# Performance work log

Measured on AMD Instinct MI355X. Metric: run time of the kernel, lower is better.

## Reference

```python
import jax, jax.numpy as jnp
import numpy as np

# Static taxonomy layout (closed over; mirrors __init__ args La/layers)
LAYER_SIZES = (100, 1000, 5000, 13900)
LAYER_STARTS = tuple(int(s) for s in np.cumsum((0,) + LAYER_SIZES)[:-1])
N_NODES = int(sum(LAYER_SIZES))
H = len(LAYER_SIZES)
BATCH = 4096


def setup_inputs() -> dict:
    key = jax.random.key(0)
    y_pred = jax.random.normal(key, (BATCH, N_NODES), dtype=jnp.float32)

    rng = np.random.default_rng(0)
    # parents[v] = global index of v's parent in the previous layer
    parents = np.zeros(N_NODES, np.int32)
    for l in range(1, H):
        s, n = LAYER_STARTS[l], LAYER_SIZES[l]
        ps, pn = LAYER_STARTS[l - 1], LAYER_SIZES[l - 1]
        parents[s:s + n] = rng.integers(ps, ps + pn, size=n)

    # hierarchy-consistent one-hot targets: pick a leaf, mark it and all ancestors
    leaf = rng.integers(LAYER_STARTS[H - 1], N_NODES, size=BATCH)
    y_true = np.zeros((BATCH, N_NODES), np.float32)
    node = leaf
    rows = np.arange(BATCH)
    for l in range(H - 1, 0, -1):
        y_true[rows, node] = 1.0
        node = parents[node]
    y_true[rows, node] = 1.0  # layer-0 ancestor

    alpha_layer = jnp.array([0.0, 1.0, 1.0, 1.0], dtype=jnp.float32)
    return {
        "y_pred": y_pred,
        "y_true": jnp.asarray(y_true),
        "parents": jnp.asarray(parents),
        "alpha_layer": alpha_layer,
    }


def reference(y_pred, y_true, parents, alpha_layer):
    # Fused, batched version of the per-sample / per-layer Python loops.
    loss = jnp.float32(0.0)
    for l in range(1, H):  # small static loop over taxonomy layers
        s, n = LAYER_STARTS[l], LAYER_SIZES[l]
        ps, pn = LAYER_STARTS[l - 1], LAYER_SIZES[l - 1]

        logits = y_pred[:, s:s + n]                      # [B, n_l]
        p = jax.nn.softmax(logits, axis=1)               # outer softmax (as in source)
        # nn.CrossEntropyLoss with probability targets == -sum(t * log_softmax(input));
        # the source feeds the already-softmaxed p (double softmax) -> reproduce exactly.
        cce = -jnp.sum(y_true[:, s:s + n] * jax.nn.log_softmax(p, axis=1), axis=1)  # [B]

        # hierarchical dependency: child prob must not exceed its parent's prob
        pp = jax.nn.softmax(y_pred[:, ps:ps + pn], axis=1)   # [B, n_{l-1}]
        pidx = parents[s:s + n] - ps                         # local parent ids [n_l]
        d = jnp.mean(jax.nn.relu(p - pp[:, pidx]), axis=1)   # [B]

        loss = loss + jnp.mean(cce + d) * alpha_layer[l]
    return loss
```

## Files before the change

kernel.cpp:

```cpp
#include <hip/hip_runtime.h>
#include <math.h>

#define BATCH   4096
#define N_NODES 20000
#define H       4
#define BLOCK   512
#define NW      (BLOCK / 64)

__device__ __forceinline__ float waveSum(float v) {
#pragma unroll
    for (int off = 32; off > 0; off >>= 1) v += __shfl_xor(v, off);
    return v;
}

__device__ __forceinline__ float bf2f(ushort h) {
    return __uint_as_float(((unsigned)h) << 16);
}
__device__ __forceinline__ ushort f2bf_trunc(float x) {
    return (ushort)(__float_as_uint(x) >> 16);
}

__global__ __launch_bounds__(BLOCK, 8) void tax_main(
    const float* __restrict__ y_pred,
    const float* __restrict__ y_true,
    const int*   __restrict__ parents,
    const float* __restrict__ alpha,
    float*       __restrict__ partial)
{
    constexpr int LSTART[H] = {0, 100, 1100, 6100};
    constexpr int LSIZE[H]  = {100, 1000, 5000, 13900};

    __shared__ __align__(8) ushort row_bf[N_NODES];
    __shared__ float sc[NW * 13 + 16];
    __shared__ float invZ_s[H];
    __shared__ float aD_s[H];
    __shared__ float contrib_s[H];

    const int tid = threadIdx.x;
    const int b   = blockIdx.x;
    const int wid = tid >> 6;
    const int lid = tid & 63;

    const float4* yp4 = reinterpret_cast<const float4*>(y_pred + (size_t)b * N_NODES);
    const float4* yt4 = reinterpret_cast<const float4*>(y_true + (size_t)b * N_NODES);

#pragma unroll
    for (int l = 0; l < H; ++l) {
        const int sq = LSTART[l] / 4, nq = LSIZE[l] / 4;
        float z = 0.f, q2 = 0.f, dt = 0.f, ys = 0.f;
        for (int i = tid; i < nq; i += BLOCK) {
            float4 v = yp4[sq + i];
            float e0 = __expf(v.x), e1 = __expf(v.y);
            float e2 = __expf(v.z), e3 = __expf(v.w);
            ushort4 h;
            h.x = f2bf_trunc(e0); h.y = f2bf_trunc(e1);
            h.z = f2bf_trunc(e2); h.w = f2bf_trunc(e3);
            *reinterpret_cast<ushort4*>(&row_bf[4 * (sq + i)]) = h;
            z += (e0 + e1) + (e2 + e3);
            if (l > 0) {
                q2 += (e0 * e0 + e1 * e1) + (e2 * e2 + e3 * e3);
                float4 t = yt4[sq + i];
                dt += t.x * e0 + t.y * e1 + t.z * e2 + t.w * e3;
                ys += (t.x + t.y) + (t.z + t.w);
            }
        }
        z = waveSum(z);
        if (l > 0) { q2 = waveSum(q2); dt = waveSum(dt); ys = waveSum(ys); }
        if (lid == 0) {
            if (l == 0) {
                sc[wid * 13] = z;
            } else {
                float* p = &sc[wid * 13 + 1 + (l - 1) * 4];
                p[0] = z; p[1] = q2; p[2] = dt; p[3] = ys;
            }
        }
    }
    __syncthreads();

    if (tid < H) {
        const int l = tid;
        float z = 0.f, q2 = 0.f, dt = 0.f, ys = 0.f;
        if (l == 0) {
            for (int w = 0; w < NW; ++w) z += sc[w * 13];
        } else {
            for (int w = 0; w < NW; ++w) {
                const float* p = &sc[w * 13 + 1 + (l - 1) * 4];
                z += p[0]; q2 += p[1]; dt += p[2]; ys += p[3];
            }
        }
        float invZ = 1.f / z;
        invZ_s[l] = invZ;
        float al = alpha[l];
        if (l > 0) {
            float S = (float)(LSIZE[l] + 1) + 0.5f * q2 * invZ * invZ;
            contrib_s[l] = al * (logf(S) * ys - dt * invZ);
        } else {
            contrib_s[l] = 0.f;
        }
        aD_s[l] = al / (float)LSIZE[l];
    }
    __syncthreads();

#pragma unroll
    for (int l = 1; l < H; ++l) {
        const int s = LSTART[l], nq = LSIZE[l] / 4;
        const float invZ  = invZ_s[l];
        const float invZp = invZ_s[l - 1];
        const int4* pa4 = reinterpret_cast<const int4*>(parents + s);

        float D = 0.f;
        for (int i = tid; i < nq; i += BLOCK) {
            ushort4 h  = *reinterpret_cast<const ushort4*>(&row_bf[s + 4 * i]);
            int4    pa = pa4[i];
            float p0 = bf2f(h.x) * invZ;
            float p1 = bf2f(h.y) * invZ;
            float p2 = bf2f(h.z) * invZ;
            float p3 = bf2f(h.w) * invZ;
            float pp0 = bf2f(row_bf[pa.x]) * invZp;
            float pp1 = bf2f(row_bf[pa.y]) * invZp;
            float pp2 = bf2f(row_bf[pa.z]) * invZp;
            float pp3 = bf2f(row_bf[pa.w]) * invZp;
            D += fmaxf(p0 - pp0, 0.f) + fmaxf(p1 - pp1, 0.f)
               + fmaxf(p2 - pp2, 0.f) + fmaxf(p3 - pp3, 0.f);
        }
        D = waveSum(D);
        if (lid == 0) sc[wid * 4 + (l - 1)] = D;
    }
    __syncthreads();

    if (tid == 0) {
        float loss = contrib_s[1] + contrib_s[2] + contrib_s[3];
#pragma unroll
        for (int l = 1; l < H; ++l) {
            float Dl = 0.f;
            for (int w = 0; w < NW; ++w) Dl += sc[w * 4 + (l - 1)];
            loss += aD_s[l] * Dl;
        }
        partial[b] = loss;
    }
}

__global__ __launch_bounds__(1024) void tax_reduce(
    const float* __restrict__ partial, float* __restrict__ out)
{
    __shared__ float red[16];
    const int tid = threadIdx.x, wid = tid >> 6, lid = tid & 63;
    float v = 0.f;
    for (int i = tid; i < BATCH; i += 1024) v += partial[i];
    v = waveSum(v);
    if (lid == 0) red[wid] = v;
    __syncthreads();
    if (wid == 0) {
        float x = (lid < 16) ? red[lid] : 0.f;
        x = waveSum(x);
        if (lid == 0) out[0] = x * (1.0f / (float)BATCH);
    }
}

extern "C" void kernel_launch(void* const* d_in, const int* in_sizes, int n_in,
                              void* d_out, int out_size, void* d_ws, size_t ws_size,
                              hipStream_t stream) {
    const float* y_pred  = (const float*)d_in[0];
    const float* y_true  = (const float*)d_in[1];
    const int*   parents = (const int*)d_in[2];
    const float* alpha   = (const float*)d_in[3];
    float* partial = (float*)d_ws;
    float* out     = (float*)d_out;

    tax_main<<<dim3(BATCH), dim3(BLOCK), 0, stream>>>(y_pred, y_true, parents, alpha, partial);
    tax_reduce<<<dim3(1), dim3(1024), 0, stream>>>(partial, out);
}
```

Before: 131.0 us.

## Process four rows per block, fusing next row's exp pass with previous row's dependency pass

```diff
diff --git a/kernel.cpp b/kernel.cpp
--- a/kernel.cpp
+++ b/kernel.cpp
@@ -6,18 +6,90 @@
 #define H       4
 #define BLOCK   512
 #define NW      (BLOCK / 64)
+#define ROWS    4
+#define GRID    (BATCH / ROWS)
+
+constexpr int LSTART_C[H] = {0, 100, 1100, 6100};
+constexpr int LSIZE_C[H]  = {100, 1000, 5000, 13900};
 
 __device__ __forceinline__ float waveSum(float v) {
 #pragma unroll
     for (int off = 32; off > 0; off >>= 1) v += __shfl_xor(v, off);
     return v;
 }
-
 __device__ __forceinline__ float bf2f(ushort h) {
     return __uint_as_float(((unsigned)h) << 16);
 }
 __device__ __forceinline__ ushort f2bf_trunc(float x) {
     return (ushort)(__float_as_uint(x) >> 16);
+}
+
+template<int L>
+__device__ __forceinline__ void p1_layer(const float4* yp4, const float4* yt4,
+    ushort* row_bf, float& z, float& q2, float& dt, float& ys, int tid)
+{
+    constexpr int SQ = LSTART_C[L] / 4, NQ = LSIZE_C[L] / 4;
+    for (int i = tid; i < NQ; i += BLOCK) {
+        float4 v = yp4[SQ + i];
+        float e0 = __expf(v.x), e1 = __expf(v.y), e2 = __expf(v.z), e3 = __expf(v.w);
+        ushort4 h;
+        h.x = f2bf_trunc(e0); h.y = f2bf_trunc(e1);
+        h.z = f2bf_trunc(e2); h.w = f2bf_trunc(e3);
+        *reinterpret_cast<ushort4*>(&row_bf[4 * (SQ + i)]) = h;
+        z += (e0 + e1) + (e2 + e3);
+        if constexpr (L > 0) {
+            q2 += (e0*e0 + e1*e1) + (e2*e2 + e3*e3);
+            float4 t = yt4[SQ + i];
+            dt += t.x*e0 + t.y*e1 + t.z*e2 + t.w*e3;
+            ys += (t.x + t.y) + (t.z + t.w);
+        }
+    }
+}
+
+template<int L>
+__device__ __forceinline__ void p2_layer(const int4* pa4, const ushort* row_bf,
+    const float* invZ_s, float& D, int tid)
+{
+    constexpr int S = LSTART_C[L], SQ = S / 4, NQ = LSIZE_C[L] / 4;
+    const float invZ = invZ_s[L], invZp = invZ_s[L - 1];
+    for (int i = tid; i < NQ; i += BLOCK) {
+        ushort4 h = *reinterpret_cast<const ushort4*>(&row_bf[S + 4 * i]);
+        int4 pa = pa4[SQ + i];
+        float p0 = bf2f(h.x)*invZ, p1 = bf2f(h.y)*invZ;
+        float p2 = bf2f(h.z)*invZ, p3 = bf2f(h.w)*invZ;
+        float pp0 = bf2f(row_bf[pa.x])*invZp, pp1 = bf2f(row_bf[pa.y])*invZp;
+        float pp2 = bf2f(row_bf[pa.z])*invZp, pp3 = bf2f(row_bf[pa.w])*invZp;
+        D += (fmaxf(p0-pp0,0.f)+fmaxf(p1-pp1,0.f)) + (fmaxf(p2-pp2,0.f)+fmaxf(p3-pp3,0.f));
+    }
+}
+
+template<int L>
+__device__ __forceinline__ void fused_layer(const float4* yp4n, const float4* yt4n,
+    const int4* pa4, ushort* row_bf, const float* invZ_s,
+    float& z, float& q2, float& dt, float& ys, float& D, int tid)
+{
+    constexpr int S = LSTART_C[L], SQ = S / 4, NQ = LSIZE_C[L] / 4;
+    const float invZ = invZ_s[L], invZp = invZ_s[L - 1];
+    for (int i = tid; i < NQ; i += BLOCK) {
+        float4 v = yp4n[SQ + i];
+        float4 t = yt4n[SQ + i];
+        int4  pa = pa4[SQ + i];
+        ushort4 h = *reinterpret_cast<const ushort4*>(&row_bf[S + 4 * i]);
+        float p0 = bf2f(h.x)*invZ, p1 = bf2f(h.y)*invZ;
+        float p2 = bf2f(h.z)*invZ, p3 = bf2f(h.w)*invZ;
+        float pp0 = bf2f(row_bf[pa.x])*invZp, pp1 = bf2f(row_bf[pa.y])*invZp;
+        float pp2 = bf2f(row_bf[pa.z])*invZp, pp3 = bf2f(row_bf[pa.w])*invZp;
+        D += (fmaxf(p0-pp0,0.f)+fmaxf(p1-pp1,0.f)) + (fmaxf(p2-pp2,0.f)+fmaxf(p3-pp3,0.f));
+        float e0 = __expf(v.x), e1 = __expf(v.y), e2 = __expf(v.z), e3 = __expf(v.w);
+        ushort4 hn;
+        hn.x = f2bf_trunc(e0); hn.y = f2bf_trunc(e1);
+        hn.z = f2bf_trunc(e2); hn.w = f2bf_trunc(e3);
+        *reinterpret_cast<ushort4*>(&row_bf[S + 4 * i]) = hn;
+        z  += (e0 + e1) + (e2 + e3);
+        q2 += (e0*e0 + e1*e1) + (e2*e2 + e3*e3);
+        dt += t.x*e0 + t.y*e1 + t.z*e2 + t.w*e3;
+        ys += (t.x + t.y) + (t.z + t.w);
+    }
 }
 
 __global__ __launch_bounds__(BLOCK, 8) void tax_main(
@@ -27,116 +99,117 @@
     const float* __restrict__ alpha,
     float*       __restrict__ partial)
 {
-    constexpr int LSTART[H] = {0, 100, 1100, 6100};
-    constexpr int LSIZE[H]  = {100, 1000, 5000, 13900};
-
     __shared__ __align__(8) ushort row_bf[N_NODES];
-    __shared__ float sc[NW * 13 + 16];
+    __shared__ float sc[NW * 20];
     __shared__ float invZ_s[H];
-    __shared__ float aD_s[H];
-    __shared__ float contrib_s[H];
+    __shared__ float contribL[H];
+    __shared__ float carry;
 
     const int tid = threadIdx.x;
-    const int b   = blockIdx.x;
     const int wid = tid >> 6;
     const int lid = tid & 63;
-
-    const float4* yp4 = reinterpret_cast<const float4*>(y_pred + (size_t)b * N_NODES);
-    const float4* yt4 = reinterpret_cast<const float4*>(y_true + (size_t)b * N_NODES);
-
-#pragma unroll
-    for (int l = 0; l < H; ++l) {
-        const int sq = LSTART[l] / 4, nq = LSIZE[l] / 4;
-        float z = 0.f, q2 = 0.f, dt = 0.f, ys = 0.f;
-        for (int i = tid; i < nq; i += BLOCK) {
-            float4 v = yp4[sq + i];
-            float e0 = __expf(v.x), e1 = __expf(v.y);
-            float e2 = __expf(v.z), e3 = __expf(v.w);
-            ushort4 h;
-            h.x = f2bf_trunc(e0); h.y = f2bf_trunc(e1);
-            h.z = f2bf_trunc(e2); h.w = f2bf_trunc(e3);
-            *reinterpret_cast<ushort4*>(&row_bf[4 * (sq + i)]) = h;
-            z += (e0 + e1) + (e2 + e3);
+    const int r0  = blockIdx.x * ROWS;
+    const int4* pa4 = reinterpret_cast<const int4*>(parents);
+
+    float z[H], q2[H], dt[H], ys[H], D[H];
+
+    auto reduce_step = [&](bool writePrev, int prevRow) {
+        float rz0 = waveSum(z[0]);
+        float r1[3], r2[3], r3[3], r4[3], rD[3];
+#pragma unroll
+        for (int l = 1; l < H; ++l) {
+            r1[l-1] = waveSum(z[l]);  r2[l-1] = waveSum(q2[l]);
+            r3[l-1] = waveSum(dt[l]); r4[l-1] = waveSum(ys[l]);
+            rD[l-1] = writePrev ? waveSum(D[l]) : 0.f;
+        }
+        if (lid == 0) {
+            float* p = &sc[wid * 20];
+            p[0] = rz0;
+#pragma unroll
+            for (int j = 0; j < 3; ++j) {
+                p[1+j] = r1[j]; p[4+j] = r2[j]; p[7+j] = r3[j];
+                p[10+j] = r4[j]; p[13+j] = rD[j];
+            }
+        }
+        __syncthreads();
+        if (tid < H) {
+            const int l = tid;
+            float zt = 0.f, q2t = 0.f, dtt = 0.f, yst = 0.f;
+            for (int w = 0; w < NW; ++w) {
+                const float* p = &sc[w * 20];
+                if (l == 0) zt += p[0];
+                else { zt += p[1+(l-1)]; q2t += p[4+(l-1)]; dtt += p[7+(l-1)]; yst += p[10+(l-1)]; }
+            }
+            float invZ = 1.f / zt;
+            invZ_s[l] = invZ;
             if (l > 0) {
-                q2 += (e0 * e0 + e1 * e1) + (e2 * e2 + e3 * e3);
-                float4 t = yt4[sq + i];
-                dt += t.x * e0 + t.y * e1 + t.z * e2 + t.w * e3;
-                ys += (t.x + t.y) + (t.z + t.w);
-            }
-        }
-        z = waveSum(z);
-        if (l > 0) { q2 = waveSum(q2); dt = waveSum(dt); ys = waveSum(ys); }
+                float S = (float)(LSIZE_C[l] + 1) + 0.5f * q2t * invZ * invZ;
+                contribL[l] = alpha[l] * (logf(S) * yst - dtt * invZ);
+            }
+        }
+        if (tid == 0 && writePrev) {
+            float acc = carry;
+#pragma unroll
+            for (int j = 0; j < 3; ++j) {
+                float Dl = 0.f;
+                for (int w = 0; w < NW; ++w) Dl += sc[w * 20 + 13 + j];
+                acc += alpha[j+1] * Dl / (float)LSIZE_C[j+1];
+            }
+            partial[prevRow] = acc;
+        }
+        __syncthreads();
+        if (tid == 0) carry = contribL[1] + contribL[2] + contribL[3];
+    };
+
+    {
+        const float4* yp4 = reinterpret_cast<const float4*>(y_pred + (size_t)r0 * N_NODES);
+        const float4* yt4 = reinterpret_cast<const float4*>(y_true + (size_t)r0 * N_NODES);
+#pragma unroll
+        for (int l = 0; l < H; ++l) { z[l]=0.f; q2[l]=0.f; dt[l]=0.f; ys[l]=0.f; D[l]=0.f; }
+        p1_layer<3>(yp4, yt4, row_bf, z[3], q2[3], dt[3], ys[3], tid);
+        p1_layer<2>(yp4, yt4, row_bf, z[2], q2[2], dt[2], ys[2], tid);
+        p1_layer<1>(yp4, yt4, row_bf, z[1], q2[1], dt[1], ys[1], tid);
+        p1_layer<0>(yp4, yt4, row_bf, z[0], q2[0], dt[0], ys[0], tid);
+    }
+    reduce_step(false, 0);
+
+#pragma unroll 1
+    for (int k = 0; k < ROWS - 1; ++k) {
+        const float4* yp4n = reinterpret_cast<const float4*>(y_pred + (size_t)(r0 + k + 1) * N_NODES);
+        const float4* yt4n = reinterpret_cast<const float4*>(y_true + (size_t)(r0 + k + 1) * N_NODES);
+#pragma unroll
+        for (int l = 0; l < H; ++l) { z[l]=0.f; q2[l]=0.f; dt[l]=0.f; ys[l]=0.f; D[l]=0.f; }
+        fused_layer<3>(yp4n, yt4n, pa4, row_bf, invZ_s, z[3], q2[3], dt[3], ys[3], D[3], tid);
+        __syncthreads();
+        fused_layer<2>(yp4n, yt4n, pa4, row_bf, invZ_s, z[2], q2[2], dt[2], ys[2], D[2], tid);
+        __syncthreads();
+        fused_layer<1>(yp4n, yt4n, pa4, row_bf, invZ_s, z[1], q2[1], dt[1], ys[1], D[1], tid);
+        __syncthreads();
+        p1_layer<0>(yp4n, yt4n, row_bf, z[0], q2[0], dt[0], ys[0], tid);
+        reduce_step(true, r0 + k);
+    }
+
+#pragma unroll
+    for (int l = 0; l < H; ++l) D[l] = 0.f;
+    p2_layer<3>(pa4, row_bf, invZ_s, D[3], tid);
+    p2_layer<2>(pa4, row_bf, invZ_s, D[2], tid);
+    p2_layer<1>(pa4, row_bf, invZ_s, D[1], tid);
+    {
+        float rD1 = waveSum(D[1]), rD2 = waveSum(D[2]), rD3 = waveSum(D[3]);
         if (lid == 0) {
-            if (l == 0) {
-                sc[wid * 13] = z;
-            } else {
-                float* p = &sc[wid * 13 + 1 + (l - 1) * 4];
-                p[0] = z; p[1] = q2; p[2] = dt; p[3] = ys;
-            }
-        }
-    }
-    __syncthreads();
-
-    if (tid < H) {
-        const int l = tid;
-        float z = 0.f, q2 = 0.f, dt = 0.f, ys = 0.f;
-        if (l == 0) {
-            for (int w = 0; w < NW; ++w) z += sc[w * 13];
-        } else {
-            for (int w = 0; w < NW; ++w) {
-                const float* p = &sc[w * 13 + 1 + (l - 1) * 4];
-                z += p[0]; q2 += p[1]; dt += p[2]; ys += p[3];
-            }
-        }
-        float invZ = 1.f / z;
-        invZ_s[l] = invZ;
-        float al = alpha[l];
-        if (l > 0) {
-            float S = (float)(LSIZE[l] + 1) + 0.5f * q2 * invZ * invZ;
-            contrib_s[l] = al * (logf(S) * ys - dt * invZ);
-        } else {
-            contrib_s[l] = 0.f;
-        }
-        aD_s[l] = al / (float)LSIZE[l];
-    }
-    __syncthreads();
-
-#pragma unroll
-    for (int l = 1; l < H; ++l) {
-        const int s = LSTART[l], nq = LSIZE[l] / 4;
-        const float invZ  = invZ_s[l];
-        const float invZp = invZ_s[l - 1];
-        const int4* pa4 = reinterpret_cast<const int4*>(parents + s);
-
-        float D = 0.f;
-        for (int i = tid; i < nq; i += BLOCK) {
-            ushort4 h  = *reinterpret_cast<const ushort4*>(&row_bf[s + 4 * i]);
-            int4    pa = pa4[i];
-            float p0 = bf2f(h.x) * invZ;
-            float p1 = bf2f(h.y) * invZ;
-            float p2 = bf2f(h.z) * invZ;
-            float p3 = bf2f(h.w) * invZ;
-            float pp0 = bf2f(row_bf[pa.x]) * invZp;
-            float pp1 = bf2f(row_bf[pa.y]) * invZp;
-            float pp2 = bf2f(row_bf[pa.z]) * invZp;
-            float pp3 = bf2f(row_bf[pa.w]) * invZp;
-            D += fmaxf(p0 - pp0, 0.f) + fmaxf(p1 - pp1, 0.f)
-               + fmaxf(p2 - pp2, 0.f) + fmaxf(p3 - pp3, 0.f);
-        }
-        D = waveSum(D);
-        if (lid == 0) sc[wid * 4 + (l - 1)] = D;
-    }
-    __syncthreads();
-
-    if (tid == 0) {
-        float loss = contrib_s[1] + contrib_s[2] + contrib_s[3];
-#pragma unroll
-        for (int l = 1; l < H; ++l) {
-            float Dl = 0.f;
-            for (int w = 0; w < NW; ++w) Dl += sc[w * 4 + (l - 1)];
-            loss += aD_s[l] * Dl;
-        }
-        partial[b] = loss;
+            sc[wid * 20 + 13] = rD1; sc[wid * 20 + 14] = rD2; sc[wid * 20 + 15] = rD3;
+        }
+        __syncthreads();
+        if (tid == 0) {
+            float acc = carry;
+#pragma unroll
+            for (int j = 0; j < 3; ++j) {
+                float Dl = 0.f;
+                for (int w = 0; w < NW; ++w) Dl += sc[w * 20 + 13 + j];
+                acc += alpha[j+1] * Dl / (float)LSIZE_C[j+1];
+            }
+            partial[r0 + ROWS - 1] = acc;
+        }
     }
 }
 
@@ -167,6 +240,6 @@
     float* partial = (float*)d_ws;
     float* out     = (float*)d_out;
 
-    tax_main<<<dim3(BATCH), dim3(BLOCK), 0, stream>>>(y_pred, y_true, parents, alpha, partial);
+    tax_main<<<dim3(GRID), dim3(BLOCK), 0, stream>>>(y_pred, y_true, parents, alpha, partial);
     tax_reduce<<<dim3(1), dim3(1024), 0, stream>>>(partial, out);
 }
```

After: 149.8 us. 1.14x slower.
